# Performance work log

Hardware: AMD Instinct MI355X
Metric: run time of the kernel (lower is better)

## Reference

```python
import jax, jax.numpy as jnp
import numpy as np

HIDDEN = 2048
HEADS = 16
HEAD_DIM = HIDDEN // HEADS  # 128
ROPE_BASE = 10000.0
RMS_EPS = 1e-6
MINUS_INF = -10000.0


def rms_norm(x, w):
    xf = x.astype(jnp.float32)
    var = jnp.mean(xf * xf, axis=-1, keepdims=True)
    return w * (x * jax.lax.rsqrt(var + RMS_EPS))


def rotate_half(x):
    x1, x2 = jnp.split(x, 2, axis=-1)
    return jnp.concatenate((-x2, x1), axis=-1)


def rope_tables(seq_len, dtype):
    inv_freq = 1.0 / (ROPE_BASE ** (jnp.arange(0, HEAD_DIM, 2, dtype=jnp.float32) / HEAD_DIM))
    t = jnp.arange(seq_len, dtype=jnp.float32)
    freqs = jnp.einsum('i,j->ij', t, inv_freq)           # [S, D/2]
    emb = jnp.concatenate((freqs, freqs), axis=-1)       # [S, D]
    return jnp.cos(emb).astype(dtype), jnp.sin(emb).astype(dtype)


def setup_inputs() -> dict:
    key = jax.random.key(0)
    ks = jax.random.split(key, 6)
    B, S, H = 2, 2048, HIDDEN
    x = jax.random.normal(ks[0], (B, S, H), dtype=jnp.float32) * 0.5
    norm_w = jnp.ones((H,), dtype=jnp.float32)
    scale = 0.02
    wq = jax.random.normal(ks[1], (H, H), dtype=jnp.float32) * scale
    wk = jax.random.normal(ks[2], (H, H), dtype=jnp.float32) * scale
    wv = jax.random.normal(ks[3], (H, H), dtype=jnp.float32) * scale
    wo = jax.random.normal(ks[4], (H, H), dtype=jnp.float32) * scale
    position_ids = jnp.broadcast_to(jnp.arange(S, dtype=jnp.int32), (B, S))
    return {"x": x, "norm_w": norm_w, "wq": wq, "wk": wk, "wv": wv,
            "wo": wo, "position_ids": position_ids}


def reference(x, norm_w, wq, wk, wv, wo, position_ids):
    B, S, H = x.shape
    h = rms_norm(x, norm_w)
    # torch Linear: y = h @ W.T, weight is [out, in]
    def proj(w):
        return jnp.einsum('bsd,od->bso', h, w).reshape(B, S, HEADS, HEAD_DIM).transpose(0, 2, 1, 3)
    q, k, v = proj(wq), proj(wk), proj(wv)  # [B, Hh, S, D]
    cos, sin = rope_tables(S, x.dtype)
    cos = cos[position_ids][:, None]  # [B, 1, S, D]
    sin = sin[position_ids][:, None]
    q = q * cos + rotate_half(q) * sin
    k = k * cos + rotate_half(k) * sin
    scores = jnp.einsum('bhqd,bhkd->bhqk', q, k) / jnp.sqrt(jnp.float32(HEAD_DIM))
    causal = jnp.tril(jnp.ones((S, S), dtype=bool))
    scores = scores + jnp.where(causal, 0.0, MINUS_INF).astype(scores.dtype)
    probs = jax.nn.softmax(scores, axis=-1)
    ctx = jnp.einsum('bhqk,bhkd->bhqd', probs, v)          # [B, Hh, S, D]
    ctx = ctx.transpose(0, 2, 1, 3).reshape(B, S, H)
    out = jnp.einsum('bsd,od->bso', ctx, wo)
    return out
```

## Files before the change

### kernel.cpp

```cpp
#include <hip/hip_runtime.h>
#include <hip/hip_bf16.h>
#include <stdint.h>

#define S_LEN   2048
#define BATCH   2
#define HID     2048
#define NHEADS  16
#define HDIM    128
#define ROWS    (BATCH * S_LEN)
#define QS      6144
#define ATT_SCALE 0.08838834764831843f

typedef __attribute__((ext_vector_type(8))) short s16x8;
typedef __attribute__((ext_vector_type(4))) float f32x4;

#define GLL16(gp, lp)                                                          \
  __builtin_amdgcn_global_load_lds(                                            \
      (__attribute__((address_space(1))) void*)(gp),                           \
      (__attribute__((address_space(3))) void*)(lp), 16, 0, 0)

__device__ __forceinline__ float bf2f(unsigned short u) {
  union { unsigned int i; float f; } v; v.i = ((unsigned int)u) << 16; return v.f;
}
__device__ __forceinline__ unsigned short f2bf(float f) {
  union { float f; unsigned int i; } v; v.f = f;
  unsigned int i = v.i;
  return (unsigned short)((i + 0x7FFFu + ((i >> 16) & 1u)) >> 16);
}
__device__ __forceinline__ void store_out(unsigned short* p, float v) { *p = f2bf(v); }
__device__ __forceinline__ void store_out(float* p, float v) { *p = v; }

__global__ __launch_bounds__(256) void cast_w_kernel(const float* __restrict__ in,
                                                     unsigned short* __restrict__ out, int n4) {
  int i = blockIdx.x * 256 + threadIdx.x;
  if (i >= n4) return;
  float4 v = ((const float4*)in)[i];
  ushort4 o;
  o.x = f2bf(v.x); o.y = f2bf(v.y); o.z = f2bf(v.z); o.w = f2bf(v.w);
  ((ushort4*)out)[i] = o;
}

__global__ __launch_bounds__(256) void rmsnorm_kernel(const float* __restrict__ x,
                                                      const float* __restrict__ w,
                                                      unsigned short* __restrict__ h) {
  int row = blockIdx.x;
  int t = threadIdx.x;
  const float4* xr4 = (const float4*)(x + (size_t)row * HID);
  float4 a = xr4[t], b = xr4[t + 256];
  float ss = a.x*a.x + a.y*a.y + a.z*a.z + a.w*a.w
           + b.x*b.x + b.y*b.y + b.z*b.z + b.w*b.w;
#pragma unroll
  for (int off = 32; off >= 1; off >>= 1) ss += __shfl_xor(ss, off, 64);
  __shared__ float red[4];
  if ((t & 63) == 0) red[t >> 6] = ss;
  __syncthreads();
  float tot = red[0] + red[1] + red[2] + red[3];
  float rs = rsqrtf(tot * (1.0f / (float)HID) + 1e-6f);
  const float4* w4 = (const float4*)w;
  float4 wa = w4[t], wb = w4[t + 256];
  ushort4 oa, ob;
  oa.x = f2bf(a.x * wa.x * rs); oa.y = f2bf(a.y * wa.y * rs);
  oa.z = f2bf(a.z * wa.z * rs); oa.w = f2bf(a.w * wa.w * rs);
  ob.x = f2bf(b.x * wb.x * rs); ob.y = f2bf(b.y * wb.y * rs);
  ob.z = f2bf(b.z * wb.z * rs); ob.w = f2bf(b.w * wb.w * rs);
  ushort4* hr = (ushort4*)(h + (size_t)row * HID);
  hr[t] = oa; hr[t + 256] = ob;
}

__global__ void rope_tab_kernel(float* __restrict__ cost, float* __restrict__ sint) {
  int s = blockIdx.x, j = threadIdx.x;
  float inv = powf(10000.0f, -((float)j) / 64.0f);
  float ang = (float)s * inv;
  cost[s * 64 + j] = cosf(ang);
  sint[s * 64 + j] = sinf(ang);
}

__global__ __launch_bounds__(256) void rope_kernel(const int* __restrict__ pos_ids,
                                                   const float* __restrict__ cost,
                                                   const float* __restrict__ sint,
                                                   unsigned short* __restrict__ qkv) {
  int row = blockIdx.x;
  int p = pos_ids[row];
  int t = threadIdx.x;
  int head = t >> 4;
  int j0 = (t & 15) * 4;
  size_t base = (size_t)row * QS + head * HDIM;
  float4 c = *(const float4*)(cost + p * 64 + j0);
  float4 s = *(const float4*)(sint + p * 64 + j0);
#pragma unroll
  for (int which = 0; which < 2; which++) {
    unsigned short* ptr = qkv + base + which * HID;
    float sc = which ? 1.0f : ATT_SCALE;
    ushort4 v1 = *(ushort4*)(ptr + j0);
    ushort4 v2 = *(ushort4*)(ptr + 64 + j0);
    ushort4 o1, o2;
    o1.x = f2bf((bf2f(v1.x) * c.x - bf2f(v2.x) * s.x) * sc);
    o1.y = f2bf((bf2f(v1.y) * c.y - bf2f(v2.y) * s.y) * sc);
    o1.z = f2bf((bf2f(v1.z) * c.z - bf2f(v2.z) * s.z) * sc);
    o1.w = f2bf((bf2f(v1.w) * c.w - bf2f(v2.w) * s.w) * sc);
    o2.x = f2bf((bf2f(v2.x) * c.x + bf2f(v1.x) * s.x) * sc);
    o2.y = f2bf((bf2f(v2.y) * c.y + bf2f(v1.y) * s.y) * sc);
    o2.z = f2bf((bf2f(v2.z) * c.z + bf2f(v1.z) * s.z) * sc);
    o2.w = f2bf((bf2f(v2.w) * c.w + bf2f(v1.w) * s.w) * sc);
    *(ushort4*)(ptr + j0) = o1;
    *(ushort4*)(ptr + 64 + j0) = o2;
  }
}

__global__ __launch_bounds__(256) void transpose_v_kernel(const unsigned short* __restrict__ qkv,
                                                          unsigned short* __restrict__ vt) {
  __shared__ unsigned short tile[64][72];
  const int stile = blockIdx.x, dt = blockIdx.y, bh = blockIdx.z;
  const int t = threadIdx.x;
  const int b = bh >> 4, h = bh & 15;
  const int s0 = stile * 64;
  const unsigned short* src = qkv + (size_t)(b * S_LEN + s0) * QS + 2 * HID + h * HDIM + dt * 64;
#pragma unroll
  for (int it = 0; it < 2; it++) {
    int sl = (t >> 3) + 32 * it;
    int dl = (t & 7) * 8;
    *(s16x8*)&tile[sl][dl] = *(const s16x8*)(src + (size_t)sl * QS + dl);
  }
  __syncthreads();
#pragma unroll
  for (int it = 0; it < 2; it++) {
    int dl = (t >> 3) + 32 * it;
    int sl8 = (t & 7) * 8;
    s16x8 o;
#pragma unroll
    for (int jj = 0; jj < 8; jj++) o[jj] = (short)tile[sl8 + jj][dl];
    *(s16x8*)(vt + (size_t)(bh * 128 + dt * 64 + dl) * S_LEN + s0 + sl8) = o;
  }
}

#define SA(kt, bi) {                                                           \
    const unsigned short* s_ = aS + (size_t)(kt) * 64;                         \
    char* d_ = (char*)Ab[bi] + tid * 16;                                       \
    GLL16(s_, d_);                                                             \
    GLL16(s_ + (size_t)64 * K, d_ + 8192);                                     \
  }
#define SB(kt, bi, hf) {                                                       \
    const unsigned short* s_ = bS + (size_t)(hf) * 128 * K + (size_t)(kt) * 64;\
    char* d_ = (char*)Bb[bi] + (hf) * 16384 + tid * 16;                        \
    GLL16(s_, d_);                                                             \
    GLL16(s_ + (size_t)64 * K, d_ + 8192);                                     \
  }

template <typename OutT, int NI>
__global__ __launch_bounds__(512, 1) void gemm8_kernel(const unsigned short* __restrict__ A,
                                                       const unsigned short* __restrict__ B,
                                                       OutT* __restrict__ C, int K, int N) {
  __shared__ __align__(16) unsigned short Ab[3][128 * 64];
  __shared__ __align__(16) unsigned short Bb[3][NI * 64 * 64];
  const int bm = blockIdx.y, bn = blockIdx.x;
  const int tid = threadIdx.x;
  const int w = tid >> 6, wr = w >> 2, wc = w & 3;
  const int l = tid & 63, g = l >> 4, r = l & 15;
  const int KT = K >> 6;

  const int srow = tid >> 3;
  const int sgr = (tid & 7) ^ (srow & 7);
  const unsigned short* aS = A + (size_t)(bm * 128 + srow) * K + sgr * 8;
  const unsigned short* bS = B + (size_t)(bn * (NI * 64) + srow) * K + sgr * 8;

  f32x4 zero = {0.f, 0.f, 0.f, 0.f};
  f32x4 acc[4][NI];
#pragma unroll
  for (int mi = 0; mi < 4; mi++)
#pragma unroll
    for (int ni = 0; ni < NI; ni++) acc[mi][ni] = zero;

  const int swx = (r & 7) << 4;
  const int ks0 = (g << 4) ^ swx;
  const int ks1 = ((4 | g) << 4) ^ swx;
  const int aOff = (wr * 64 + r) * 128;
  const int bOff = (wc * (NI * 16) + r) * 128;

  SA(0, 0); SB(0, 0, 0); if (NI == 4) SB(0, 0, 1);
  SA(1, 1); SB(1, 1, 0); if (NI == 4) SB(1, 1, 1);

  int cur = 0;
  for (int kt = 0; kt < KT; ++kt) {
    const int b2 = (cur >= 1) ? cur - 1 : cur + 2;
    if (kt == KT - 1)      { asm volatile("s_waitcnt vmcnt(0)" ::: "memory"); }
    else if (NI == 4)      { asm volatile("s_waitcnt vmcnt(6)" ::: "memory"); }
    else                   { asm volatile("s_waitcnt vmcnt(4)" ::: "memory"); }
    __builtin_amdgcn_s_barrier();
    __builtin_amdgcn_sched_barrier(0);
    const char* lA = (const char*)Ab[cur];
    const char* lB = (const char*)Bb[cur];
    const bool more = (kt + 2 < KT);

    s16x8 a[4][2], b[NI][2];
#pragma unroll
    for (int mi = 0; mi < 4; mi++) {
      a[mi][0] = *(const s16x8*)(lA + aOff + mi * 2048 + ks0);
      a[mi][1] = *(const s16x8*)(lA + aOff + mi * 2048 + ks1);
    }
#pragma unroll
    for (int ni = 0; ni < NI / 2; ni++) {
      b[ni][0] = *(const s16x8*)(lB + bOff + ni * 2048 + ks0);
      b[ni][1] = *(const s16x8*)(lB + bOff + ni * 2048 + ks1);
    }
    if (more) { SA(kt + 2, b2); if (NI == 4) SB(kt + 2, b2, 0); }
    __builtin_amdgcn_s_setprio(1);
#pragma unroll
    for (int kk = 0; kk < 2; kk++)
#pragma unroll
      for (int ni = 0; ni < NI / 2; ni++)
#pragma unroll
        for (int mi = 0; mi < 4; mi++)
          acc[mi][ni] = __builtin_amdgcn_mfma_f32_16x16x32_bf16(a[mi][kk], b[ni][kk], acc[mi][ni], 0, 0, 0);
    __builtin_amdgcn_s_setprio(0);
    __builtin_amdgcn_sched_barrier(0);

#pragma unroll
    for (int ni = NI / 2; ni < NI; ni++) {
      b[ni][0] = *(const s16x8*)(lB + bOff + ni * 2048 + ks0);
      b[ni][1] = *(const s16x8*)(lB + bOff + ni * 2048 + ks1);
    }
    if (more) { if (NI == 4) { SB(kt + 2, b2, 1); } else { SB(kt + 2, b2, 0); } }
    __builtin_amdgcn_s_setprio(1);
#pragma unroll
    for (int kk = 0; kk < 2; kk++)
#pragma unroll
      for (int ni = NI / 2; ni < NI; ni++)
#pragma unroll
        for (int mi = 0; mi < 4; mi++)
          acc[mi][ni] = __builtin_amdgcn_mfma_f32_16x16x32_bf16(a[mi][kk], b[ni][kk], acc[mi][ni], 0, 0, 0);
    __builtin_amdgcn_s_setprio(0);
    cur = (cur == 2) ? 0 : cur + 1;
  }

#pragma unroll
  for (int mi = 0; mi < 4; mi++)
#pragma unroll
    for (int ni = 0; ni < NI; ni++) {
      const int crow = bm * 128 + wr * 64 + mi * 16 + g * 4;
      const int ccol = bn * (NI * 64) + wc * (NI * 16) + ni * 16 + r;
#pragma unroll
      for (int j = 0; j < 4; j++)
        store_out(&C[(size_t)(crow + j) * N + ccol], acc[mi][ni][j]);
    }
}

__global__ __launch_bounds__(512) void attn_kernel(const unsigned short* __restrict__ QKV,
                                                   const unsigned short* __restrict__ VT,
                                                   unsigned short* __restrict__ O) {
  __shared__ __align__(16) unsigned short Ksm[2][64 * 128];
  __shared__ __align__(16) unsigned short VTsm[2][128 * 64];
  __shared__ __align__(16) unsigned short Psm[8 * 32 * 64];
  const int bid = blockIdx.x;
  const int grp = bid & 7, j = bid >> 3;
  const int bh = (grp << 2) | (j & 3);
  const int pr = j >> 2;
  const int qtA = 8 + pr, qtB = 7 - pr;
  const int b = bh >> 4, hd = bh & 15;
  const int tid = threadIdx.x, w = tid >> 6, l = tid & 63, g = l >> 4, r = l & 15;
  const int qbs = (w < 4 ? qtA : qtB) * 128 + (w & 3) * 32;

  s16x8 qf[2][4];
#pragma unroll
  for (int s = 0; s < 2; s++) {
    const unsigned short* qp = QKV + (size_t)(b * S_LEN + qbs + s * 16 + r) * QS + hd * HDIM;
#pragma unroll
    for (int ks = 0; ks < 4; ks++) qf[s][ks] = *(const s16x8*)(qp + ks * 32 + g * 8);
  }

  float mreg[2][4], lreg[2][4];
  f32x4 zero = {0.f, 0.f, 0.f, 0.f};
  f32x4 oacc[2][8];
#pragma unroll
  for (int s = 0; s < 2; s++)
#pragma unroll
    for (int jj = 0; jj < 4; jj++) { mreg[s][jj] = -1e30f; lreg[s][jj] = 0.f; }
#pragma unroll
  for (int s = 0; s < 2; s++)
#pragma unroll
    for (int di = 0; di < 8; di++) oacc[s][di] = zero;

  const int cK = tid & 15, rowK = tid >> 4;
  const unsigned short* kp_base = QKV + (size_t)(b * S_LEN + rowK) * QS + HID + hd * HDIM
                                  + ((cK ^ (rowK & 7)) << 3);
  const int cV = tid & 7, dV = tid >> 3;
  const unsigned short* vp_base = VT + (size_t)(bh * 128 + dV) * S_LEN + ((cV ^ (dV & 7)) << 3);
  char* const ksm0 = (char*)Ksm;
  char* const vtsm0 = (char*)VTsm;
  char* const psm_w = (char*)Psm + w * 4096;

#define STAGE(kt, bufi)                                                        \
  {                                                                            \
    const unsigned short* kp_ = kp_base + (size_t)((kt) * 64) * QS;            \
    const unsigned short* vp_ = vp_base + (kt) * 64;                           \
    char* kd_ = ksm0 + (bufi) * 16384;                                         \
    char* vd_ = vtsm0 + (bufi) * 16384;                                        \
    GLL16(kp_, kd_ + tid * 16);                                                \
    GLL16(kp_ + (size_t)32 * QS, kd_ + (tid + 512) * 16);                      \
    GLL16(vp_, vd_ + tid * 16);                                                \
    GLL16(vp_ + (size_t)64 * S_LEN, vd_ + (tid + 512) * 16);                   \
  }

  const int nt = 2 * qtA + 2;
  STAGE(0, 0);
  asm volatile("s_waitcnt vmcnt(0)" ::: "memory");
  __builtin_amdgcn_s_barrier();
  __builtin_amdgcn_sched_barrier(0);

  for (int kt2 = 0; kt2 < nt; kt2++) {
    const int buf = kt2 & 1;
    if (kt2 + 1 < nt) STAGE(kt2 + 1, buf ^ 1);

    const bool active = (kt2 * 64) <= (qbs + 31);
    if (active) {
      const char* ksm_c = ksm0 + buf * 16384;
      const char* vtsm_c = vtsm0 + buf * 16384;
      f32x4 sacc[2][4];
#pragma unroll
      for (int s = 0; s < 2; s++)
#pragma unroll
        for (int ni = 0; ni < 4; ni++) sacc[s][ni] = zero;
#pragma unroll
      for (int ni = 0; ni < 4; ni++) {
        const int krow = ni * 16 + r;
        const int swz = (krow & 7) << 4;
        const char* kb2 = ksm_c + krow * 256;
#pragma unroll
        for (int ks = 0; ks < 4; ks++) {
          s16x8 kf = *(const s16x8*)(kb2 + ((ks * 64 + g * 16) ^ swz));
#pragma unroll
          for (int s = 0; s < 2; s++)
            sacc[s][ni] = __builtin_amdgcn_mfma_f32_16x16x32_bf16(qf[s][ks], kf, sacc[s][ni], 0, 0, 0);
        }
      }

#pragma unroll
      for (int s = 0; s < 2; s++) {
        const int qb_s = qbs + s * 16;
        const bool domask = (kt2 * 64 + 63) > qb_s;
        float mrow[4];
#pragma unroll
        for (int jj = 0; jj < 4; jj++) mrow[jj] = -1e30f;
#pragma unroll
        for (int ni = 0; ni < 4; ni++)
#pragma unroll
          for (int jj = 0; jj < 4; jj++) {
            float sval = sacc[s][ni][jj];
            if (domask && (kt2 * 64 + ni * 16 + r) > (qb_s + g * 4 + jj)) sval = -1e30f;
            sacc[s][ni][jj] = sval;
            mrow[jj] = fmaxf(mrow[jj], sval);
          }
#pragma unroll
        for (int jj = 0; jj < 4; jj++) {
#pragma unroll
          for (int off = 8; off >= 1; off >>= 1)
            mrow[jj] = fmaxf(mrow[jj], __shfl_xor(mrow[jj], off, 64));
        }
        float corr[4];
#pragma unroll
        for (int jj = 0; jj < 4; jj++) {
          float mn = fmaxf(mreg[s][jj], mrow[jj]);
          corr[jj] = __expf(mreg[s][jj] - mn);
          mreg[s][jj] = mn;
          float sm = 0.f;
#pragma unroll
          for (int ni = 0; ni < 4; ni++) {
            float p2 = __expf(sacc[s][ni][jj] - mn);
            sacc[s][ni][jj] = p2;
            sm += p2;
          }
#pragma unroll
          for (int off = 8; off >= 1; off >>= 1) sm += __shfl_xor(sm, off, 64);
          lreg[s][jj] = lreg[s][jj] * corr[jj] + sm;
        }
#pragma unroll
        for (int di = 0; di < 8; di++)
#pragma unroll
          for (int jj = 0; jj < 4; jj++) oacc[s][di][jj] *= corr[jj];

#pragma unroll
        for (int ni = 0; ni < 4; ni++)
#pragma unroll
          for (int jj = 0; jj < 4; jj++) {
            int prow = s * 16 + g * 4 + jj;
            int byte = (prow * 128 + ((ni * 16 + r) << 1)) ^ ((prow & 7) << 4);
            *(unsigned short*)(psm_w + byte) = f2bf(sacc[s][ni][jj]);
          }
      }

#pragma unroll
      for (int ksl = 0; ksl < 2; ksl++) {
        s16x8 pa[2];
#pragma unroll
        for (int s = 0; s < 2; s++)
          pa[s] = *(const s16x8*)(psm_w + (((s * 16 + r) * 128 + ((ksl * 32 + g * 8) << 1)) ^ ((r & 7) << 4)));
        const int kgran = ksl * 4 + g;
#pragma unroll
        for (int di = 0; di < 8; di++) {
          const int d = di * 16 + r;
          s16x8 vf = *(const s16x8*)(vtsm_c + d * 128 + ((kgran ^ (d & 7)) << 4));
#pragma unroll
          for (int s = 0; s < 2; s++)
            oacc[s][di] = __builtin_amdgcn_mfma_f32_16x16x32_bf16(pa[s], vf, oacc[s][di], 0, 0, 0);
        }
      }
    }
    asm volatile("s_waitcnt vmcnt(0)" ::: "memory");
    __builtin_amdgcn_s_barrier();
    __builtin_amdgcn_sched_barrier(0);
  }
#undef STAGE

#pragma unroll
  for (int s = 0; s < 2; s++)
#pragma unroll
    for (int di = 0; di < 8; di++)
#pragma unroll
      for (int jj = 0; jj < 4; jj++) {
        int orow = qbs + s * 16 + g * 4 + jj;
        O[(size_t)(b * S_LEN + orow) * HID + hd * HDIM + di * 16 + r] =
            f2bf(oacc[s][di][jj] / lreg[s][jj]);
      }
}

extern "C" void kernel_launch(void* const* d_in, const int* in_sizes, int n_in,
                              void* d_out, int out_size, void* d_ws, size_t ws_size,
                              hipStream_t stream) {
  const float* x      = (const float*)d_in[0];
  const float* norm_w = (const float*)d_in[1];
  const float* wq     = (const float*)d_in[2];
  const float* wk     = (const float*)d_in[3];
  const float* wv     = (const float*)d_in[4];
  const float* wo     = (const float*)d_in[5];
  const int*   pos    = (const int*)d_in[6];
  float* out = (float*)d_out;

  char* ws = (char*)d_ws;
  const size_t WQKV_B = (size_t)3 * HID * HID * 2;
  const size_t VT_B   = (size_t)ROWS * HID * 2;
  const size_t H_B    = (size_t)ROWS * HID * 2;
  const size_t QKV_B  = (size_t)ROWS * QS * 2;

  unsigned short* wqkvb = (unsigned short*)(ws);
  unsigned short* vt    = (unsigned short*)(ws);
  unsigned short* wob   = (unsigned short*)(ws + VT_B);
  unsigned short* h     = (unsigned short*)(ws + WQKV_B);
  unsigned short* qkv   = (unsigned short*)(ws + WQKV_B + H_B);
  float* cost = (float*)(ws + WQKV_B + H_B + QKV_B);
  float* sint = cost + (size_t)S_LEN * 64;

  const int n4 = HID * HID / 4;
  cast_w_kernel<<<n4 / 256, 256, 0, stream>>>(wq, wqkvb, n4);
  cast_w_kernel<<<n4 / 256, 256, 0, stream>>>(wk, wqkvb + (size_t)HID * HID, n4);
  cast_w_kernel<<<n4 / 256, 256, 0, stream>>>(wv, wqkvb + (size_t)2 * HID * HID, n4);
  rope_tab_kernel<<<S_LEN, 64, 0, stream>>>(cost, sint);
  rmsnorm_kernel<<<ROWS, 256, 0, stream>>>(x, norm_w, h);

  dim3 qkvgrid(QS / 256, ROWS / 128);
  gemm8_kernel<unsigned short, 4><<<qkvgrid, 512, 0, stream>>>(h, wqkvb, qkv, HID, QS);

  cast_w_kernel<<<n4 / 256, 256, 0, stream>>>(wo, wob, n4);
  dim3 tgrid(S_LEN / 64, 2, BATCH * NHEADS);
  transpose_v_kernel<<<tgrid, 256, 0, stream>>>(qkv, vt);

  rope_kernel<<<ROWS, 256, 0, stream>>>(pos, cost, sint, qkv);

  attn_kernel<<<256, 512, 0, stream>>>(qkv, vt, h );

  dim3 ogrid(HID / 128, ROWS / 128);
  gemm8_kernel<float, 2><<<ogrid, 512, 0, stream>>>(h, wob, out, HID, HID);
}
```

Measured before the change: 307.2 us.

## Restructure attention into smaller single-buffered blocks with heaviest query tiles first

```diff
diff --git a/kernel.cpp b/kernel.cpp
--- a/kernel.cpp
+++ b/kernel.cpp
@@ -244,182 +244,154 @@
     }
 }
 
-__global__ __launch_bounds__(512) void attn_kernel(const unsigned short* __restrict__ QKV,
-                                                   const unsigned short* __restrict__ VT,
-                                                   unsigned short* __restrict__ O) {
-  __shared__ __align__(16) unsigned short Ksm[2][64 * 128];
-  __shared__ __align__(16) unsigned short VTsm[2][128 * 64];
-  __shared__ __align__(16) unsigned short Psm[8 * 32 * 64];
+__global__ __launch_bounds__(256, 4) void attn_kernel(const unsigned short* __restrict__ QKV,
+                                                      const unsigned short* __restrict__ VT,
+                                                      unsigned short* __restrict__ O) {
+  __shared__ __align__(16) unsigned short Ksm[64 * 128];
+  __shared__ __align__(16) unsigned short VTsm[128 * 64];
+  __shared__ __align__(16) unsigned short Psm[4 * 16 * 64];
   const int bid = blockIdx.x;
-  const int grp = bid & 7, j = bid >> 3;
-  const int bh = (grp << 2) | (j & 3);
-  const int pr = j >> 2;
-  const int qtA = 8 + pr, qtB = 7 - pr;
+  const int grp = bid & 7, idx = bid >> 3;
+  const int qt = 31 - (idx >> 2);
+  const int bh = (grp << 2) | (idx & 3);
   const int b = bh >> 4, hd = bh & 15;
   const int tid = threadIdx.x, w = tid >> 6, l = tid & 63, g = l >> 4, r = l & 15;
-  const int qbs = (w < 4 ? qtA : qtB) * 128 + (w & 3) * 32;
-
-  s16x8 qf[2][4];
-#pragma unroll
-  for (int s = 0; s < 2; s++) {
-    const unsigned short* qp = QKV + (size_t)(b * S_LEN + qbs + s * 16 + r) * QS + hd * HDIM;
-#pragma unroll
-    for (int ks = 0; ks < 4; ks++) qf[s][ks] = *(const s16x8*)(qp + ks * 32 + g * 8);
-  }
-
-  float mreg[2][4], lreg[2][4];
+  const int qbs = qt * 64 + w * 16;
+
+  const unsigned short* qp = QKV + (size_t)(b * S_LEN + qbs + r) * QS + hd * HDIM;
+  s16x8 qf[4];
+#pragma unroll
+  for (int ks = 0; ks < 4; ks++) qf[ks] = *(const s16x8*)(qp + ks * 32 + g * 8);
+
+  float mreg[4], lreg[4];
   f32x4 zero = {0.f, 0.f, 0.f, 0.f};
-  f32x4 oacc[2][8];
-#pragma unroll
-  for (int s = 0; s < 2; s++)
-#pragma unroll
-    for (int jj = 0; jj < 4; jj++) { mreg[s][jj] = -1e30f; lreg[s][jj] = 0.f; }
-#pragma unroll
-  for (int s = 0; s < 2; s++)
-#pragma unroll
-    for (int di = 0; di < 8; di++) oacc[s][di] = zero;
+  f32x4 oacc[8];
+#pragma unroll
+  for (int jj = 0; jj < 4; jj++) { mreg[jj] = -1e30f; lreg[jj] = 0.f; }
+#pragma unroll
+  for (int di = 0; di < 8; di++) oacc[di] = zero;
 
   const int cK = tid & 15, rowK = tid >> 4;
   const unsigned short* kp_base = QKV + (size_t)(b * S_LEN + rowK) * QS + HID + hd * HDIM
                                   + ((cK ^ (rowK & 7)) << 3);
   const int cV = tid & 7, dV = tid >> 3;
   const unsigned short* vp_base = VT + (size_t)(bh * 128 + dV) * S_LEN + ((cV ^ (dV & 7)) << 3);
-  char* const ksm0 = (char*)Ksm;
-  char* const vtsm0 = (char*)VTsm;
-  char* const psm_w = (char*)Psm + w * 4096;
-
-#define STAGE(kt, bufi)                                                        \
+  char* const ksm_c = (char*)Ksm;
+  char* const vtsm_c = (char*)VTsm;
+  char* const psm_w = (char*)Psm + w * 2048;
+
+#define STAGE(kt)                                                              \
   {                                                                            \
     const unsigned short* kp_ = kp_base + (size_t)((kt) * 64) * QS;            \
     const unsigned short* vp_ = vp_base + (kt) * 64;                           \
-    char* kd_ = ksm0 + (bufi) * 16384;                                         \
-    char* vd_ = vtsm0 + (bufi) * 16384;                                        \
-    GLL16(kp_, kd_ + tid * 16);                                                \
-    GLL16(kp_ + (size_t)32 * QS, kd_ + (tid + 512) * 16);                      \
-    GLL16(vp_, vd_ + tid * 16);                                                \
-    GLL16(vp_ + (size_t)64 * S_LEN, vd_ + (tid + 512) * 16);                   \
-  }
-
-  const int nt = 2 * qtA + 2;
-  STAGE(0, 0);
-  asm volatile("s_waitcnt vmcnt(0)" ::: "memory");
-  __builtin_amdgcn_s_barrier();
-  __builtin_amdgcn_sched_barrier(0);
+    GLL16(kp_,                      ksm_c + tid * 16);                         \
+    GLL16(kp_ + (size_t)16 * QS,    ksm_c + (tid + 256) * 16);                 \
+    GLL16(kp_ + (size_t)32 * QS,    ksm_c + (tid + 512) * 16);                 \
+    GLL16(kp_ + (size_t)48 * QS,    ksm_c + (tid + 768) * 16);                 \
+    GLL16(vp_,                      vtsm_c + tid * 16);                        \
+    GLL16(vp_ + (size_t)32 * S_LEN, vtsm_c + (tid + 256) * 16);                \
+    GLL16(vp_ + (size_t)64 * S_LEN, vtsm_c + (tid + 512) * 16);                \
+    GLL16(vp_ + (size_t)96 * S_LEN, vtsm_c + (tid + 768) * 16);                \
+  }
+
+  const int nt = qt + 1;
+  STAGE(0);
 
   for (int kt2 = 0; kt2 < nt; kt2++) {
-    const int buf = kt2 & 1;
-    if (kt2 + 1 < nt) STAGE(kt2 + 1, buf ^ 1);
-
-    const bool active = (kt2 * 64) <= (qbs + 31);
-    if (active) {
-      const char* ksm_c = ksm0 + buf * 16384;
-      const char* vtsm_c = vtsm0 + buf * 16384;
-      f32x4 sacc[2][4];
-#pragma unroll
-      for (int s = 0; s < 2; s++)
-#pragma unroll
-        for (int ni = 0; ni < 4; ni++) sacc[s][ni] = zero;
-#pragma unroll
-      for (int ni = 0; ni < 4; ni++) {
-        const int krow = ni * 16 + r;
-        const int swz = (krow & 7) << 4;
-        const char* kb2 = ksm_c + krow * 256;
-#pragma unroll
-        for (int ks = 0; ks < 4; ks++) {
-          s16x8 kf = *(const s16x8*)(kb2 + ((ks * 64 + g * 16) ^ swz));
-#pragma unroll
-          for (int s = 0; s < 2; s++)
-            sacc[s][ni] = __builtin_amdgcn_mfma_f32_16x16x32_bf16(qf[s][ks], kf, sacc[s][ni], 0, 0, 0);
-        }
-      }
-
-#pragma unroll
-      for (int s = 0; s < 2; s++) {
-        const int qb_s = qbs + s * 16;
-        const bool domask = (kt2 * 64 + 63) > qb_s;
-        float mrow[4];
-#pragma unroll
-        for (int jj = 0; jj < 4; jj++) mrow[jj] = -1e30f;
-#pragma unroll
-        for (int ni = 0; ni < 4; ni++)
-#pragma unroll
-          for (int jj = 0; jj < 4; jj++) {
-            float sval = sacc[s][ni][jj];
-            if (domask && (kt2 * 64 + ni * 16 + r) > (qb_s + g * 4 + jj)) sval = -1e30f;
-            sacc[s][ni][jj] = sval;
-            mrow[jj] = fmaxf(mrow[jj], sval);
-          }
-#pragma unroll
-        for (int jj = 0; jj < 4; jj++) {
-#pragma unroll
-          for (int off = 8; off >= 1; off >>= 1)
-            mrow[jj] = fmaxf(mrow[jj], __shfl_xor(mrow[jj], off, 64));
-        }
-        float corr[4];
-#pragma unroll
-        for (int jj = 0; jj < 4; jj++) {
-          float mn = fmaxf(mreg[s][jj], mrow[jj]);
-          corr[jj] = __expf(mreg[s][jj] - mn);
-          mreg[s][jj] = mn;
-          float sm = 0.f;
-#pragma unroll
-          for (int ni = 0; ni < 4; ni++) {
-            float p2 = __expf(sacc[s][ni][jj] - mn);
-            sacc[s][ni][jj] = p2;
-            sm += p2;
-          }
-#pragma unroll
-          for (int off = 8; off >= 1; off >>= 1) sm += __shfl_xor(sm, off, 64);
-          lreg[s][jj] = lreg[s][jj] * corr[jj] + sm;
-        }
-#pragma unroll
-        for (int di = 0; di < 8; di++)
-#pragma unroll
-          for (int jj = 0; jj < 4; jj++) oacc[s][di][jj] *= corr[jj];
-
-#pragma unroll
-        for (int ni = 0; ni < 4; ni++)
-#pragma unroll
-          for (int jj = 0; jj < 4; jj++) {
-            int prow = s * 16 + g * 4 + jj;
-            int byte = (prow * 128 + ((ni * 16 + r) << 1)) ^ ((prow & 7) << 4);
-            *(unsigned short*)(psm_w + byte) = f2bf(sacc[s][ni][jj]);
-          }
-      }
-
-#pragma unroll
-      for (int ksl = 0; ksl < 2; ksl++) {
-        s16x8 pa[2];
-#pragma unroll
-        for (int s = 0; s < 2; s++)
-          pa[s] = *(const s16x8*)(psm_w + (((s * 16 + r) * 128 + ((ksl * 32 + g * 8) << 1)) ^ ((r & 7) << 4)));
-        const int kgran = ksl * 4 + g;
-#pragma unroll
-        for (int di = 0; di < 8; di++) {
-          const int d = di * 16 + r;
-          s16x8 vf = *(const s16x8*)(vtsm_c + d * 128 + ((kgran ^ (d & 7)) << 4));
-#pragma unroll
-          for (int s = 0; s < 2; s++)
-            oacc[s][di] = __builtin_amdgcn_mfma_f32_16x16x32_bf16(pa[s], vf, oacc[s][di], 0, 0, 0);
-        }
-      }
-    }
     asm volatile("s_waitcnt vmcnt(0)" ::: "memory");
     __builtin_amdgcn_s_barrier();
     __builtin_amdgcn_sched_barrier(0);
+
+    f32x4 sacc[4];
+#pragma unroll
+    for (int ni = 0; ni < 4; ni++) sacc[ni] = zero;
+#pragma unroll
+    for (int ni = 0; ni < 4; ni++) {
+      const int krow = ni * 16 + r;
+      const int swz = (krow & 7) << 4;
+      const char* kb2 = ksm_c + krow * 256;
+#pragma unroll
+      for (int ks = 0; ks < 4; ks++) {
+        s16x8 kf = *(const s16x8*)(kb2 + ((ks * 64 + g * 16) ^ swz));
+        sacc[ni] = __builtin_amdgcn_mfma_f32_16x16x32_bf16(qf[ks], kf, sacc[ni], 0, 0, 0);
+      }
+    }
+
+    const bool domask = (kt2 == qt);
+    float mrow[4];
+#pragma unroll
+    for (int jj = 0; jj < 4; jj++) mrow[jj] = -1e30f;
+#pragma unroll
+    for (int ni = 0; ni < 4; ni++)
+#pragma unroll
+      for (int jj = 0; jj < 4; jj++) {
+        float sval = sacc[ni][jj];
+        if (domask && (kt2 * 64 + ni * 16 + r) > (qbs + g * 4 + jj)) sval = -1e30f;
+        sacc[ni][jj] = sval;
+        mrow[jj] = fmaxf(mrow[jj], sval);
+      }
+#pragma unroll
+    for (int jj = 0; jj < 4; jj++) {
+#pragma unroll
+      for (int off = 8; off >= 1; off >>= 1)
+        mrow[jj] = fmaxf(mrow[jj], __shfl_xor(mrow[jj], off, 64));
+    }
+    float corr[4];
+#pragma unroll
+    for (int jj = 0; jj < 4; jj++) {
+      float mn = fmaxf(mreg[jj], mrow[jj]);
+      corr[jj] = __expf(mreg[jj] - mn);
+      mreg[jj] = mn;
+      float sm = 0.f;
+#pragma unroll
+      for (int ni = 0; ni < 4; ni++) {
+        float p2 = __expf(sacc[ni][jj] - mn);
+        sacc[ni][jj] = p2;
+        sm += p2;
+      }
+#pragma unroll
+      for (int off = 8; off >= 1; off >>= 1) sm += __shfl_xor(sm, off, 64);
+      lreg[jj] = lreg[jj] * corr[jj] + sm;
+    }
+#pragma unroll
+    for (int di = 0; di < 8; di++)
+#pragma unroll
+      for (int jj = 0; jj < 4; jj++) oacc[di][jj] *= corr[jj];
+
+#pragma unroll
+    for (int ni = 0; ni < 4; ni++)
+#pragma unroll
+      for (int jj = 0; jj < 4; jj++) {
+        int prow = g * 4 + jj;
+        int byte = (prow * 128 + ((ni * 16 + r) << 1)) ^ ((prow & 7) << 4);
+        *(unsigned short*)(psm_w + byte) = f2bf(sacc[ni][jj]);
+      }
+
+#pragma unroll
+    for (int ksl = 0; ksl < 2; ksl++) {
+      s16x8 pa = *(const s16x8*)(psm_w + ((r * 128 + ((ksl * 32 + g * 8) << 1)) ^ ((r & 7) << 4)));
+      const int kgran = ksl * 4 + g;
+#pragma unroll
+      for (int di = 0; di < 8; di++) {
+        const int d = di * 16 + r;
+        s16x8 vf = *(const s16x8*)(vtsm_c + d * 128 + ((kgran ^ (d & 7)) << 4));
+        oacc[di] = __builtin_amdgcn_mfma_f32_16x16x32_bf16(pa, vf, oacc[di], 0, 0, 0);
+      }
+    }
+
+    __builtin_amdgcn_s_barrier();
+    if (kt2 + 1 < nt) STAGE(kt2 + 1);
   }
 #undef STAGE
 
 #pragma unroll
-  for (int s = 0; s < 2; s++)
-#pragma unroll
-    for (int di = 0; di < 8; di++)
-#pragma unroll
-      for (int jj = 0; jj < 4; jj++) {
-        int orow = qbs + s * 16 + g * 4 + jj;
-        O[(size_t)(b * S_LEN + orow) * HID + hd * HDIM + di * 16 + r] =
-            f2bf(oacc[s][di][jj] / lreg[s][jj]);
-      }
+  for (int di = 0; di < 8; di++)
+#pragma unroll
+    for (int jj = 0; jj < 4; jj++) {
+      int orow = qbs + g * 4 + jj;
+      O[(size_t)(b * S_LEN + orow) * HID + hd * HDIM + di * 16 + r] =
+          f2bf(oacc[di][jj] / lreg[jj]);
+    }
 }
 
 extern "C" void kernel_launch(void* const* d_in, const int* in_sizes, int n_in,
@@ -464,7 +436,7 @@
 
   rope_kernel<<<ROWS, 256, 0, stream>>>(pos, cost, sint, qkv);
 
-  attn_kernel<<<256, 512, 0, stream>>>(qkv, vt, h );
+  attn_kernel<<<1024, 256, 0, stream>>>(qkv, vt, h );
 
   dim3 ogrid(HID / 128, ROWS / 128);
   gemm8_kernel<float, 2><<<ogrid, 512, 0, stream>>>(h, wob, out, HID, HID);
```

Result: faster. 298.2 us (-2.9%).
